# Kernel tuning notes

Measured on AMD Instinct MI355X. Metric: run time of the kernel, lower is better.

Reference implementation:

```python
import jax, jax.numpy as jnp
import numpy as np

EMB = 64          # emb_size
LG = 64           # lg_msg_dim
NDB = 16          # num_dist_basis
NCB = 16          # num_cos_basis
NCLS = 40
NLAYERS = 2
NJK = NLAYERS + 2  # jumping-knowledge sequence length
HID = (NJK * EMB) // 2  # PyG JK-LSTM hidden size = 128


def setup_inputs() -> dict:
    key = jax.random.key(0)
    ks = jax.random.split(key, 24)
    N, Eg, Elg, F = 50000, 800000, 800000, 128
    s = 0.05
    inp = {
        "x": jax.random.normal(ks[0], (N, F), jnp.float32),
        "edge_index_g": jax.random.randint(ks[1], (2, Eg), 0, N, jnp.int32),
        "edge_attr_g": jax.random.uniform(ks[2], (Eg, NDB), jnp.float32),
        "edge_index_lg": jax.random.randint(ks[3], (2, Elg), 0, Eg, jnp.int32),
        "edge_attr_lg": jax.random.uniform(ks[4], (Elg, NCB), jnp.float32),
        # parameters (nn.Linear convention: W is [out, in])
        "W_feat": jax.random.normal(ks[5], (EMB, F), jnp.float32) * s,
        "W_msg": jax.random.normal(ks[6], (LG, 2 * EMB + NDB), jnp.float32) * s,
        "W_lg2g": jax.random.normal(ks[7], (EMB, LG), jnp.float32) * s,
        "b_lg2g": jax.random.normal(ks[8], (EMB,), jnp.float32) * s,
        "W_msg_layers": jax.random.normal(ks[9], (NLAYERS, LG, 2 * LG + NCB), jnp.float32) * s,
        # bidirectional LSTM params (PyTorch gate order i,f,g,o)
        "Wih_f": jax.random.normal(ks[10], (4 * HID, EMB), jnp.float32) * s,
        "Whh_f": jax.random.normal(ks[11], (4 * HID, HID), jnp.float32) * s,
        "bih_f": jax.random.normal(ks[12], (4 * HID,), jnp.float32) * s,
        "bhh_f": jax.random.normal(ks[13], (4 * HID,), jnp.float32) * s,
        "Wih_b": jax.random.normal(ks[14], (4 * HID, EMB), jnp.float32) * s,
        "Whh_b": jax.random.normal(ks[15], (4 * HID, HID), jnp.float32) * s,
        "bih_b": jax.random.normal(ks[16], (4 * HID,), jnp.float32) * s,
        "bhh_b": jax.random.normal(ks[17], (4 * HID,), jnp.float32) * s,
        "W_att": jax.random.normal(ks[18], (1, 2 * HID), jnp.float32) * s,
        "b_att": jax.random.normal(ks[19], (1,), jnp.float32) * s,
        "W_out": jax.random.normal(ks[20], (NCLS, EMB), jnp.float32) * s,
    }
    return inp


def _lstm(x_seq, Wih, Whh, bih, bhh, reverse):
    # x_seq: [N, L, C] -> hs: [N, L, H]
    N = x_seq.shape[0]
    H = Whh.shape[1]
    b = bih + bhh

    def step(carry, x_t):
        h, c = carry
        gates = x_t @ Wih.T + h @ Whh.T + b
        i, f, g, o = jnp.split(gates, 4, axis=-1)
        c = jax.nn.sigmoid(f) * c + jax.nn.sigmoid(i) * jnp.tanh(g)
        h = jax.nn.sigmoid(o) * jnp.tanh(c)
        return (h, c), h

    xs = jnp.swapaxes(x_seq, 0, 1)  # [L, N, C]
    init = (jnp.zeros((N, H), x_seq.dtype), jnp.zeros((N, H), x_seq.dtype))
    _, hs = jax.lax.scan(step, init, xs, reverse=reverse)
    return jnp.swapaxes(hs, 0, 1)


def reference(x, edge_index_g, edge_attr_g, edge_index_lg, edge_attr_lg,
              W_feat, W_msg, W_lg2g, b_lg2g, W_msg_layers,
              Wih_f, Whh_f, bih_f, bhh_f, Wih_b, Whh_b, bih_b, bhh_b,
              W_att, b_att, W_out):
    N = x.shape[0]
    Eg = edge_attr_g.shape[0]
    seg = jax.ops.segment_sum

    # node embedding (eval mode: dropout is identity)
    node_emb = jax.nn.relu(x @ W_feat.T)  # [N, EMB]

    # initial linegraph node features: gather endpoints -> concat -> linear -> relu
    m1 = node_emb[edge_index_g[0]]  # [Eg, EMB]
    m2 = node_emb[edge_index_g[1]]
    msg_emb = jax.nn.relu(jnp.concatenate([m1, m2, edge_attr_g], -1) @ W_msg.T)  # [Eg, LG]

    node_embs = [node_emb]
    msg_red = msg_emb @ W_lg2g.T + b_lg2g
    node_embs.append(seg(msg_red, edge_index_g[1], num_segments=N))

    # message-passing layers on the linegraph
    for l in range(W_msg_layers.shape[0]):
        s = msg_emb[edge_index_lg[0]]
        d = msg_emb[edge_index_lg[1]]
        m = jax.nn.relu(jnp.concatenate([s, d, edge_attr_lg], -1) @ W_msg_layers[l].T)
        msg_emb = seg(m, edge_index_lg[1], num_segments=Eg)  # scatter_add over linegraph
        incoming = seg(msg_emb, edge_index_g[1], num_segments=N)
        node_embs.append(incoming @ W_lg2g.T + b_lg2g)

    # JumpingKnowledge ('lstm'): bidirectional LSTM -> attention -> weighted sum
    x_jk = jnp.stack(node_embs, axis=1)  # [N, NJK, EMB]
    h_f = _lstm(x_jk, Wih_f, Whh_f, bih_f, bhh_f, reverse=False)
    h_b = _lstm(x_jk, Wih_b, Whh_b, bih_b, bhh_b, reverse=True)
    h = jnp.concatenate([h_f, h_b], -1)  # [N, NJK, 2*HID]
    alpha = jax.nn.softmax((h @ W_att.T + b_att)[..., 0], axis=-1)  # [N, NJK]
    final_emb = jnp.sum(x_jk * alpha[..., None], axis=1)  # [N, EMB]

    out = final_emb @ W_out.T
    return jax.nn.log_softmax(out, axis=-1)
```

## Files before the change

### kernel.cpp

```cpp
#include <hip/hip_runtime.h>

typedef unsigned short u16;
typedef unsigned int u32;
typedef __attribute__((ext_vector_type(8))) short bf16x8;
typedef __attribute__((ext_vector_type(4))) float f32x4;

#define MFMA(a, b, c) __builtin_amdgcn_mfma_f32_16x16x32_bf16(a, b, c, 0, 0, 0)

__device__ __forceinline__ u16 f2bf(float x) {
    union { float f; u32 u; } v; v.f = x;
    u32 r = (v.u + 0x7FFFu + ((v.u >> 16) & 1u)) >> 16;
    return (u16)r;
}
__device__ __forceinline__ float bf2f(u16 b) {
    union { u32 u; float f; } v; v.u = ((u32)b) << 16;
    return v.f;
}
__device__ __forceinline__ void casAddPair(u32* w, float lo, float hi) {
    u32 old = *w, assumed;
    do {
        assumed = old;
        u32 des = (u32)f2bf(bf2f((u16)(assumed & 0xFFFFu)) + lo) |
                  ((u32)f2bf(bf2f((u16)(assumed >> 16)) + hi) << 16);
        if (des == assumed) break;
        old = atomicCAS(w, assumed, des);
    } while (old != assumed);
}

__global__ __launch_bounds__(256) void prep_w(
    const float* __restrict__ Whh_f, const float* __restrict__ Whh_b,
    const float* __restrict__ Wih_f, const float* __restrict__ Wih_b,
    const float* __restrict__ bih_f, const float* __restrict__ bhh_f,
    const float* __restrict__ bih_b, const float* __restrict__ bhh_b,
    const float* __restrict__ W_feat, const float* __restrict__ W_msg,
    const float* __restrict__ W_msg_l, const float* __restrict__ W_lg2g,
    u16* __restrict__ WhhB, u16* __restrict__ WihB, float* __restrict__ BS,
    u16* __restrict__ WfeatB, u16* __restrict__ WmsgB,
    u16* __restrict__ WmsgLB, u16* __restrict__ Wlg2gB)
{
    const float L2E = 1.4426950408889634f;
    int i = blockIdx.x * 256 + threadIdx.x;
    if (i < 131072) {
        int d = i >> 16, r = i & 65535;
        float s = (((r >> 14) & 3) == 2) ? 2.f * L2E : L2E;
        WhhB[i] = f2bf(s * (d ? Whh_b[r] : Whh_f[r]));
    } else if (i < 196608) {
        int i2 = i - 131072; int d = i2 >> 15, r = i2 & 32767;
        float s = (((r >> 13) & 3) == 2) ? 2.f * L2E : L2E;
        WihB[i2] = f2bf(s * (d ? Wih_b[r] : Wih_f[r]));
    } else if (i < 197632) {
        int i3 = i - 196608; int d = i3 >> 9, g = i3 & 511;
        float s = (((g >> 7) & 3) == 2) ? 2.f * L2E : L2E;
        BS[i3] = s * (d ? (bih_b[g] + bhh_b[g]) : (bih_f[g] + bhh_f[g]));
    } else if (i < 205824) {
        int j = i - 197632; WfeatB[j] = f2bf(W_feat[j]);
    } else if (i < 215040) {
        int j = i - 205824; WmsgB[j] = f2bf(W_msg[j]);
    } else if (i < 233472) {
        int j = i - 215040; WmsgLB[j] = f2bf(W_msg_l[j]);
    } else if (i < 237568) {
        int j = i - 233472; Wlg2gB[j] = f2bf(W_lg2g[j]);
    }
}

__global__ __launch_bounds__(256) void count_kernel(const int* __restrict__ dst,
                                                    u32* __restrict__ cnt, long E)
{
    long i = (long)blockIdx.x * 256 + threadIdx.x;
    if (i < E) atomicAdd(&cnt[dst[i]], 1u);
}

__global__ __launch_bounds__(256) void scan1(const u32* __restrict__ a,
                                             u32* __restrict__ part, int n)
{
    __shared__ u32 ts[256];
    int b = blockIdx.x, t = threadIdx.x;
    long i0 = (long)b * 1024 + t * 4;
    u32 s = 0;
#pragma unroll
    for (int k = 0; k < 4; ++k) { long i = i0 + k; if (i < n) s += a[i]; }
    ts[t] = s; __syncthreads();
    for (int off = 1; off < 256; off <<= 1) {
        u32 x = (t >= off) ? ts[t - off] : 0u;
        __syncthreads(); ts[t] += x; __syncthreads();
    }
    if (t == 255) part[b] = ts[255];
}

__global__ __launch_bounds__(1024) void scan2(u32* __restrict__ part, int nb,
                                              u32* __restrict__ total_out)
{
    __shared__ u32 ts[1024];
    int t = threadIdx.x;
    u32 v = (t < nb) ? part[t] : 0u;
    ts[t] = v; __syncthreads();
    for (int off = 1; off < 1024; off <<= 1) {
        u32 x = (t >= off) ? ts[t - off] : 0u;
        __syncthreads(); ts[t] += x; __syncthreads();
    }
    if (t < nb) part[t] = ts[t] - v;
    if (t == 1023 && total_out) *total_out = ts[1023];
}

__global__ __launch_bounds__(256) void scan3(u32* __restrict__ a,
                                             const u32* __restrict__ part, int n)
{
    __shared__ u32 ts[256];
    int b = blockIdx.x, t = threadIdx.x;
    long i0 = (long)b * 1024 + t * 4;
    u32 v[4]; u32 s = 0;
#pragma unroll
    for (int k = 0; k < 4; ++k) { long i = i0 + k; v[k] = (i < n) ? a[i] : 0u; s += v[k]; }
    ts[t] = s; __syncthreads();
    for (int off = 1; off < 256; off <<= 1) {
        u32 x = (t >= off) ? ts[t - off] : 0u;
        __syncthreads(); ts[t] += x; __syncthreads();
    }
    u32 run = part[b] + ts[t] - s;
#pragma unroll
    for (int k = 0; k < 4; ++k) {
        long i = i0 + k;
        if (i < n) { u32 x = v[k]; a[i] = run; run += x; }
    }
}

__global__ __launch_bounds__(256) void fill_kernel(const int* __restrict__ dst,
                                                   u32* __restrict__ off,
                                                   int* __restrict__ list, long E)
{
    long i = (long)blockIdx.x * 256 + threadIdx.x;
    if (i < E) {
        u32 pos = atomicAdd(&off[dst[i]], 1u);
        list[pos] = (int)i;
    }
}

__global__ __launch_bounds__(256) void zero_fill(const u32* __restrict__ offc,
                                                 u16* __restrict__ outb, long NB)
{
    long idx = (long)blockIdx.x * 256 + threadIdx.x;
    long n = idx >> 3; int q = (int)(idx & 7);
    if (n >= NB) return;
    u32 s = n ? offc[n - 1] : 0u;
    u32 e = offc[n];
    bool need = (s == e) || ((s >> 7) != ((e - 1) >> 7));
    if (need) *(uint4*)(outb + n * 64 + q * 8) = make_uint4(0, 0, 0, 0);
}

template <int K, bool RELU, bool INBF16>
__global__ __launch_bounds__(256) void rowgemm(
    const void* __restrict__ in, const u16* __restrict__ W,
    const float* __restrict__ bias, const float* __restrict__ bias_scale,
    u16* __restrict__ outb, int M)
{
    constexpr int KP = K + 8;
    constexpr int K8 = K / 8;
    __shared__ u16 inS[64 * KP];
    __shared__ u16 WS[64 * KP];
    int t = threadIdx.x;
    long rb = (long)blockIdx.x * 64;
    for (int i = t; i < 64 * K8; i += 256) {
        int c = i / K8, q = i - c * K8;
        *(uint4*)&WS[c * KP + q * 8] = *(const uint4*)&W[c * K + q * 8];
    }
    if (INBF16) {
        const u16* inb = (const u16*)in;
        for (int i = t; i < 64 * K8; i += 256) {
            int r = i / K8, q = i - r * K8;
            long gr = rb + r;
            uint4 v = make_uint4(0, 0, 0, 0);
            if (gr < M) v = *(const uint4*)&inb[gr * (long)K + q * 8];
            *(uint4*)&inS[r * KP + q * 8] = v;
        }
    } else {
        const float* inf = (const float*)in;
        for (int i = t; i < 64 * K; i += 256) {
            int r = i / K, k = i - r * K;
            long gr = rb + r;
            inS[r * KP + k] = (gr < M) ? f2bf(inf[gr * (long)K + k]) : (u16)0;
        }
    }
    __syncthreads();
    int l = t & 63, w = t >> 6, lr = l & 15, lq = l >> 4;
    f32x4 acc[4];
#pragma unroll
    for (int i = 0; i < 4; ++i) acc[i] = (f32x4){0.f, 0.f, 0.f, 0.f};
#pragma unroll
    for (int kc = 0; kc < K; kc += 32) {
        bf16x8 a = *(const bf16x8*)&inS[(w * 16 + lr) * KP + kc + lq * 8];
#pragma unroll
        for (int ct = 0; ct < 4; ++ct) {
            bf16x8 b = *(const bf16x8*)&WS[(ct * 16 + lr) * KP + kc + lq * 8];
            acc[ct] = MFMA(a, b, acc[ct]);
        }
    }
#pragma unroll
    for (int ct = 0; ct < 4; ++ct)
#pragma unroll
        for (int r = 0; r < 4; ++r) {
            long gr = rb + w * 16 + lq * 4 + r;
            if (gr < M) {
                int c = ct * 16 + lr;
                float v = acc[ct][r];
                if (bias) v += bias[c] * (bias_scale ? bias_scale[gr] : 1.f);
                if (RELU) v = fmaxf(v, 0.f);
                outb[gr * 64 + c] = f2bf(v);
            }
        }
}

__global__ __launch_bounds__(512, 4) void edge_msg_init2(
    const u16* __restrict__ feat, const int* __restrict__ ei,
    const float* __restrict__ attr, const u16* __restrict__ W,
    u16* __restrict__ outb, long E)
{
    __shared__ u16 WS[64 * 168];
    __shared__ u16 eds[128 * 64];
    int t = threadIdx.x;
    long eb = (long)blockIdx.x * 128;
    for (int i = t; i < 1152; i += 512) {
        int c = i / 18, q = i - c * 18;
        *(uint4*)&WS[c * 168 + q * 8] = *(const uint4*)&W[c * 144 + q * 8];
    }
    if (t < 192) {
        int c = t / 3, q = t - c * 3;
        *(uint4*)&WS[c * 168 + 144 + q * 8] = make_uint4(0, 0, 0, 0);
    }
    int w = t >> 6, l = t & 63, lr = l & 15, lq = l >> 4;
    long e = eb + w * 16 + lr;
    long ec = (e < E) ? e : (E - 1);
    int src = ei[ec], dst = ei[E + ec];
    bf16x8 A[5];
    {
        const uint4* sp = (const uint4*)(feat + (long)src * 64);
        const uint4* dp = (const uint4*)(feat + (long)dst * 64);
        *(uint4*)&A[0] = sp[lq];
        *(uint4*)&A[1] = sp[4 + lq];
        *(uint4*)&A[2] = dp[lq];
        *(uint4*)&A[3] = dp[4 + lq];
        uint4 pv = make_uint4(0, 0, 0, 0);
        if (lq < 2) {
            const float4* ap = (const float4*)(attr + ec * 16) + lq * 2;
            float4 b0 = ap[0], b1 = ap[1];
            pv.x = (u32)f2bf(b0.x) | ((u32)f2bf(b0.y) << 16);
            pv.y = (u32)f2bf(b0.z) | ((u32)f2bf(b0.w) << 16);
            pv.z = (u32)f2bf(b1.x) | ((u32)f2bf(b1.y) << 16);
            pv.w = (u32)f2bf(b1.z) | ((u32)f2bf(b1.w) << 16);
        }
        *(uint4*)&A[4] = pv;
    }
    __syncthreads();
    f32x4 acc[4];
#pragma unroll
    for (int ct = 0; ct < 4; ++ct) acc[ct] = (f32x4){0.f, 0.f, 0.f, 0.f};
#pragma unroll
    for (int kc = 0; kc < 5; ++kc) {
#pragma unroll
        for (int ct = 0; ct < 4; ++ct) {
            bf16x8 b = *(const bf16x8*)&WS[(ct * 16 + lr) * 168 + kc * 32 + lq * 8];
            acc[ct] = MFMA(A[kc], b, acc[ct]);
        }
    }
#pragma unroll
    for (int ct = 0; ct < 4; ++ct)
#pragma unroll
        for (int r = 0; r < 4; ++r) {
            int row = w * 16 + lq * 4 + r;
            int col = ct * 16 + lr;
            eds[row * 64 + col] = f2bf(fmaxf(acc[ct][r], 0.f));
        }
    __syncthreads();
    for (int j = t; j < 1024; j += 512) {
        int le = j >> 3, q = j & 7;
        long e2 = eb + le;
        if (e2 < E)
            *(uint4*)(outb + e2 * 64 + q * 8) = *(const uint4*)&eds[le * 64 + q * 8];
    }
}

__global__ __launch_bounds__(512, 4) void edge_msg_lg2(
    const u16* __restrict__ feat, const int* __restrict__ ei,
    const float* __restrict__ attr, const u16* __restrict__ W,
    const int* __restrict__ list, u16* __restrict__ outb, long E)
{
    __shared__ u16 WS[64 * 168];
    __shared__ u16 eds[128 * 64];
    __shared__ int dstS[128];
    __shared__ int idS[128];
    __shared__ int srcS[128];
    __shared__ int dprevS, dnextS;
    int t = threadIdx.x;
    long pb = (long)blockIdx.x * 128;
    for (int i = t; i < 1152; i += 512) {
        int c = i / 18, q = i - c * 18;
        *(uint4*)&WS[c * 168 + q * 8] = *(const uint4*)&W[c * 144 + q * 8];
    }
    if (t < 192) {
        int c = t / 3, q = t - c * 3;
        *(uint4*)&WS[c * 168 + 144 + q * 8] = make_uint4(0, 0, 0, 0);
    }
    if (t < 128) {
        long p = pb + t;
        int id = (p < E) ? list[p] : -1;
        idS[t] = id;
        srcS[t] = (id >= 0) ? ei[id] : 0;
        dstS[t] = (id >= 0) ? ei[E + id] : -1;
    } else if (t == 128) {
        dprevS = (pb > 0) ? ei[E + list[pb - 1]] : -2;
    } else if (t == 129) {
        dnextS = (pb + 128 < E) ? ei[E + list[pb + 128]] : -2;
    }
    __syncthreads();
    int w = t >> 6, l = t & 63, lr = l & 15, lq = l >> 4;
    int el = w * 16 + lr;
    int id = idS[el];
    long idc = (id >= 0) ? (long)id : 0;
    int src = srcS[el];
    int dst = (dstS[el] >= 0) ? dstS[el] : 0;
    bf16x8 A[5];
    {
        const uint4* sp = (const uint4*)(feat + (long)src * 64);
        const uint4* dp = (const uint4*)(feat + (long)dst * 64);
        *(uint4*)&A[0] = sp[lq];
        *(uint4*)&A[1] = sp[4 + lq];
        *(uint4*)&A[2] = dp[lq];
        *(uint4*)&A[3] = dp[4 + lq];
        uint4 pv = make_uint4(0, 0, 0, 0);
        if (lq < 2) {
            const float4* ap = (const float4*)(attr + idc * 16) + lq * 2;
            float4 b0 = ap[0], b1 = ap[1];
            pv.x = (u32)f2bf(b0.x) | ((u32)f2bf(b0.y) << 16);
            pv.y = (u32)f2bf(b0.z) | ((u32)f2bf(b0.w) << 16);
            pv.z = (u32)f2bf(b1.x) | ((u32)f2bf(b1.y) << 16);
            pv.w = (u32)f2bf(b1.z) | ((u32)f2bf(b1.w) << 16);
        }
        *(uint4*)&A[4] = pv;
    }
    f32x4 acc[4];
#pragma unroll
    for (int ct = 0; ct < 4; ++ct) acc[ct] = (f32x4){0.f, 0.f, 0.f, 0.f};
#pragma unroll
    for (int kc = 0; kc < 5; ++kc) {
#pragma unroll
        for (int ct = 0; ct < 4; ++ct) {
            bf16x8 b = *(const bf16x8*)&WS[(ct * 16 + lr) * 168 + kc * 32 + lq * 8];
            acc[ct] = MFMA(A[kc], b, acc[ct]);
        }
    }
#pragma unroll
    for (int ct = 0; ct < 4; ++ct)
#pragma unroll
        for (int r = 0; r < 4; ++r) {
            int row = w * 16 + lq * 4 + r;
            int col = ct * 16 + lr;
            eds[row * 64 + col] = f2bf(fmaxf(acc[ct][r], 0.f));
        }
    __syncthreads();
    for (int j = t; j < 4096; j += 512) {
        int le = j >> 5, wd = j & 31;
        int d = dstS[le];
        if (d < 0) continue;
        if (le > 0 && dstS[le - 1] == d) continue;
        float lo = 0.f, hi = 0.f;
        int le2 = le;
        do {
            u32 pair = *(const u32*)&eds[le2 * 64 + wd * 2];
            lo += bf2f((u16)(pair & 0xFFFFu));
            hi += bf2f((u16)(pair >> 16));
            ++le2;
        } while (le2 < 128 && dstS[le2] == d);
        bool bprev = (le == 0 && dprevS == d);
        bool bnext = (le2 == 128 && dnextS == d);
        u32* dw = (u32*)(outb + (long)d * 64 + wd * 2);
        if (bprev || bnext) {
            casAddPair(dw, lo, hi);
        } else {
            *dw = (u32)f2bf(lo) | ((u32)f2bf(hi) << 16);
        }
    }
}

__global__ __launch_bounds__(256) void gather_gw(
    const u16* __restrict__ m, const int* __restrict__ list,
    const u32* __restrict__ offc, const u16* __restrict__ Wg,
    const float* __restrict__ bias, int useDeg,
    u16* __restrict__ outb, int N)
{
    __shared__ u16 WS[64 * 66];
    __shared__ float aggS[4][64];
    __shared__ float degS[4];
    int t = threadIdx.x;
    for (int i = t; i < 4096; i += 256) {
        int r = i >> 6, k = i & 63;
        WS[k * 66 + r] = Wg[i];
    }
    int wv = t >> 6, l = t & 63, c = l & 31, half = l >> 5;
    long n = (long)blockIdx.x * 4 + wv;
    long nn = (n < N) ? n : (long)(N - 1);
    u32 start = nn ? offc[nn - 1] : 0u;
    u32 end = offc[nn];
    float s0 = 0.f, s1 = 0.f;
    for (u32 i = start + half; i < end; i += 2) {
        int e = list[i];
        u32 pair = *(const u32*)&m[(long)e * 64 + c * 2];
        s0 += bf2f((u16)(pair & 0xFFFFu));
        s1 += bf2f((u16)(pair >> 16));
    }
    s0 += __shfl_xor(s0, 32);
    s1 += __shfl_xor(s1, 32);
    if (half == 0) { aggS[wv][c * 2] = s0; aggS[wv][c * 2 + 1] = s1; }
    if (l == 0) degS[wv] = (float)(end - start);
    __syncthreads();
    float acc = 0.f;
#pragma unroll 8
    for (int k = 0; k < 64; ++k)
        acc += aggS[wv][k] * bf2f(WS[k * 66 + l]);
    float scale = useDeg ? degS[wv] : 1.f;
    acc += bias[l] * scale;
    if (n < N) outb[n * 64 + l] = f2bf(acc);
}

__global__ __launch_bounds__(512, 2) void lstm3(
    const u16* __restrict__ jkB, const u16* __restrict__ WhhB,
    const u16* __restrict__ WihB, const float* __restrict__ BS,
    const float* __restrict__ Watt, float* __restrict__ scores,
    int N)
{
    __shared__ u16 hS[64 * 136];
    __shared__ u16 xS[2][64 * 72];
    __shared__ float bsS[512];
    __shared__ float part[4 * 64 * 8];
    int t = threadIdx.x;
    int dir = blockIdx.y;
    int w = t >> 6, l = t & 63, lr = l & 15, lq = l >> 4;
    const u16* WhhD = WhhB + (long)dir * 65536;
    const u16* WihD = WihB + (long)dir * 32768;
    long n0 = (long)blockIdx.x * 64;
    int pn = t >> 3, pj = t & 7;
    long pgn = n0 + pn;

    {
        int tt0 = dir ? 3 : 0;
        uint4 v = make_uint4(0, 0, 0, 0);
        if (pgn < N) v = *(const uint4*)&jkB[((long)tt0 * N + pgn) * 64 + pj * 8];
        *(uint4*)&xS[0][pn * 72 + pj * 8] = v;
    }
    bsS[t] = BS[dir * 512 + t];

    int grow0 = w * 16 + lq * 4;
    bf16x8 Wh[4][4];
#pragma unroll
    for (int ty = 0; ty < 4; ++ty) {
        int g = ty * 128 + w * 16 + lr;
#pragma unroll
        for (int kc = 0; kc < 4; ++kc)
            Wh[ty][kc] = *(const bf16x8*)&WhhD[g * 128 + kc * 32 + lq * 8];
    }
    const u16* pWiBase = WihD + (w * 16 + lr) * 64 + lq * 8;
    float4 Wa4 = *(const float4*)&Watt[dir * 128 + grow0];
    float* scOut = scores + (long)dir * N * 4;

    float creg[4][4] = {};
    __syncthreads();

#pragma unroll 1
    for (int s = 0; s < 4; ++s) {
        int tt = dir ? (3 - s) : s;
        int cur = s & 1;
        uint4 xpre;
        if (s < 3) {
            int ttn = dir ? (2 - s) : (s + 1);
            xpre = make_uint4(0, 0, 0, 0);
            if (pgn < N) xpre = *(const uint4*)&jkB[((long)ttn * N + pgn) * 64 + pj * 8];
        }
        const u16* pW = pWiBase;
        asm volatile("" : "+v"(pW));
        float u[4][4];
        {
            bf16x8 wi0 = *(const bf16x8*)(pW);
            bf16x8 wi1 = *(const bf16x8*)(pW + 32);
            bf16x8 wg0 = *(const bf16x8*)(pW + 16384);
            bf16x8 wg1 = *(const bf16x8*)(pW + 16416);
            f32x4 bi = *(const f32x4*)&bsS[grow0];
            f32x4 bg = *(const f32x4*)&bsS[256 + grow0];
            f32x4 acc[2][4];
#pragma unroll
            for (int nt = 0; nt < 4; ++nt) { acc[0][nt] = bi; acc[1][nt] = bg; }
            if (s) {
#pragma unroll
                for (int kc = 0; kc < 4; ++kc) {
                    bf16x8 a[4];
#pragma unroll
                    for (int nt = 0; nt < 4; ++nt)
                        a[nt] = *(const bf16x8*)&hS[(nt * 16 + lr) * 136 + kc * 32 + lq * 8];
#pragma unroll
                    for (int nt = 0; nt < 4; ++nt) {
                        acc[0][nt] = MFMA(Wh[0][kc], a[nt], acc[0][nt]);
                        acc[1][nt] = MFMA(Wh[2][kc], a[nt], acc[1][nt]);
                    }
                }
            }
#pragma unroll
            for (int kc = 0; kc < 2; ++kc) {
                bf16x8 wi = kc ? wi1 : wi0;
                bf16x8 wg = kc ? wg1 : wg0;
                bf16x8 a[4];
#pragma unroll
                for (int nt = 0; nt < 4; ++nt)
                    a[nt] = *(const bf16x8*)&xS[cur][(nt * 16 + lr) * 72 + kc * 32 + lq * 8];
#pragma unroll
                for (int nt = 0; nt < 4; ++nt) {
                    acc[0][nt] = MFMA(wi, a[nt], acc[0][nt]);
                    acc[1][nt] = MFMA(wg, a[nt], acc[1][nt]);
                }
            }
#pragma unroll
            for (int nt = 0; nt < 4; ++nt)
#pragma unroll
                for (int r = 0; r < 4; ++r) {
                    float si = __builtin_amdgcn_rcpf(
                        1.f + __builtin_amdgcn_exp2f(-acc[0][nt][r]));
                    float tg = 2.f * __builtin_amdgcn_rcpf(
                        1.f + __builtin_amdgcn_exp2f(-acc[1][nt][r])) - 1.f;
                    u[nt][r] = si * tg;
                }
        }
        {
            bf16x8 wf0 = *(const bf16x8*)(pW + 8192);
            bf16x8 wf1 = *(const bf16x8*)(pW + 8224);
            bf16x8 wo0 = *(const bf16x8*)(pW + 24576);
            bf16x8 wo1 = *(const bf16x8*)(pW + 24608);
            f32x4 bfv = *(const f32x4*)&bsS[128 + grow0];
            f32x4 bov = *(const f32x4*)&bsS[384 + grow0];
            f32x4 acc[2][4];
#pragma unroll
            for (int nt = 0; nt < 4; ++nt) { acc[0][nt] = bfv; acc[1][nt] = bov; }
            if (s) {
#pragma unroll
                for (int kc = 0; kc < 4; ++kc) {
                    bf16x8 a[4];
#pragma unroll
                    for (int nt = 0; nt < 4; ++nt)
                        a[nt] = *(const bf16x8*)&hS[(nt * 16 + lr) * 136 + kc * 32 + lq * 8];
#pragma unroll
                    for (int nt = 0; nt < 4; ++nt) {
                        acc[0][nt] = MFMA(Wh[1][kc], a[nt], acc[0][nt]);
                        acc[1][nt] = MFMA(Wh[3][kc], a[nt], acc[1][nt]);
                    }
                }
            }
#pragma unroll
            for (int kc = 0; kc < 2; ++kc) {
                bf16x8 wf = kc ? wf1 : wf0;
                bf16x8 wo = kc ? wo1 : wo0;
                bf16x8 a[4];
#pragma unroll
                for (int nt = 0; nt < 4; ++nt)
                    a[nt] = *(const bf16x8*)&xS[cur][(nt * 16 + lr) * 72 + kc * 32 + lq * 8];
#pragma unroll
                for (int nt = 0; nt < 4; ++nt) {
                    acc[0][nt] = MFMA(wf, a[nt], acc[0][nt]);
                    acc[1][nt] = MFMA(wo, a[nt], acc[1][nt]);
                }
            }
            if (s) __syncthreads();
#pragma unroll
            for (int nt = 0; nt < 4; ++nt) {
                float hv[4];
#pragma unroll
                for (int r = 0; r < 4; ++r) {
                    float sf = __builtin_amdgcn_rcpf(
                        1.f + __builtin_amdgcn_exp2f(-acc[0][nt][r]));
                    float c = sf * creg[nt][r] + u[nt][r];
                    float so = __builtin_amdgcn_rcpf(
                        1.f + __builtin_amdgcn_exp2f(-acc[1][nt][r]));
                    float th = 2.f * __builtin_amdgcn_rcpf(
                        1.f + __builtin_amdgcn_exp2f(-2.8853900817779268f * c)) - 1.f;
                    creg[nt][r] = c;
                    hv[r] = so * th;
                }
                float p = hv[0] * Wa4.x + hv[1] * Wa4.y + hv[2] * Wa4.z + hv[3] * Wa4.w;
                p += __shfl_xor(p, 16);
                p += __shfl_xor(p, 32);
                if (lq == 0) part[(tt * 64 + nt * 16 + lr) * 8 + w] = p;
                if (s < 3) {
                    u32 p0, p1;
                    asm("v_cvt_pk_bf16_f32 %0, %1, %2" : "=v"(p0) : "v"(hv[0]), "v"(hv[1]));
                    asm("v_cvt_pk_bf16_f32 %0, %1, %2" : "=v"(p1) : "v"(hv[2]), "v"(hv[3]));
                    *(uint2*)&hS[(nt * 16 + lr) * 136 + grow0] = make_uint2(p0, p1);
                }
            }
        }
        if (s < 3) {
            *(uint4*)&xS[cur ^ 1][pn * 72 + pj * 8] = xpre;
            __syncthreads();
        }
    }
    __syncthreads();
    if (t < 256) {
        int tt = t >> 6, node = t & 63;
        long gn = n0 + node;
        if (gn < N) {
            const float4* pp = (const float4*)&part[(tt * 64 + node) * 8];
            float4 a = pp[0], b = pp[1];
            scOut[gn * 4 + tt] = a.x + a.y + a.z + a.w + b.x + b.y + b.z + b.w;
        }
    }
}

__global__ __launch_bounds__(256) void final_kernel(
    const u16* __restrict__ jkB, const float* __restrict__ scores,
    const float* __restrict__ Wout, float* __restrict__ out, int N)
{
    __shared__ float feS[4][64];
    int t = threadIdx.x, l = t & 63, w = t >> 6;
    long n = (long)blockIdx.x * 4 + w;
    bool ok = (n < N);
    long nn = ok ? n : (long)(N - 1);
    float sc[4];
#pragma unroll
    for (int tt = 0; tt < 4; ++tt)
        sc[tt] = scores[nn * 4 + tt] + scores[(long)N * 4 + nn * 4 + tt];
    float m = fmaxf(fmaxf(sc[0], sc[1]), fmaxf(sc[2], sc[3]));
    float e0 = __expf(sc[0] - m), e1 = __expf(sc[1] - m);
    float e2 = __expf(sc[2] - m), e3 = __expf(sc[3] - m);
    float den = e0 + e1 + e2 + e3;
    float a0 = e0 / den, a1 = e1 / den, a2 = e2 / den, a3 = e3 / den;
    float fe = a0 * bf2f(jkB[nn * 64 + l]) + a1 * bf2f(jkB[((long)N + nn) * 64 + l]) +
               a2 * bf2f(jkB[((long)2 * N + nn) * 64 + l]) +
               a3 * bf2f(jkB[((long)3 * N + nn) * 64 + l]);
    feS[w][l] = fe;
    __syncthreads();
    float logit = 0.f;
    if (l < 40)
        for (int c = 0; c < 64; ++c) logit += feS[w][c] * Wout[l * 64 + c];
    float v = (l < 40) ? logit : -1e30f;
    for (int off = 32; off; off >>= 1) v = fmaxf(v, __shfl_xor(v, off));
    float ex = (l < 40) ? __expf(logit - v) : 0.f;
    for (int off = 32; off; off >>= 1) ex += __shfl_xor(ex, off);
    if (ok && l < 40) out[n * 40 + l] = logit - v - __logf(ex);
}

extern "C" void kernel_launch(void* const* d_in, const int* in_sizes, int n_in,
                              void* d_out, int out_size, void* d_ws, size_t ws_size,
                              hipStream_t stream)
{
    const float* x        = (const float*)d_in[0];
    const int*   eig      = (const int*)d_in[1];
    const float* eag      = (const float*)d_in[2];
    const int*   eilg     = (const int*)d_in[3];
    const float* ealg     = (const float*)d_in[4];
    const float* W_feat   = (const float*)d_in[5];
    const float* W_msg    = (const float*)d_in[6];
    const float* W_lg2g   = (const float*)d_in[7];
    const float* b_lg2g   = (const float*)d_in[8];
    const float* W_msg_l  = (const float*)d_in[9];
    const float* Wih_f    = (const float*)d_in[10];
    const float* Whh_f    = (const float*)d_in[11];
    const float* bih_f    = (const float*)d_in[12];
    const float* bhh_f    = (const float*)d_in[13];
    const float* Wih_b    = (const float*)d_in[14];
    const float* Whh_b    = (const float*)d_in[15];
    const float* bih_b    = (const float*)d_in[16];
    const float* bhh_b    = (const float*)d_in[17];
    const float* W_att    = (const float*)d_in[18];
    const float* W_out    = (const float*)d_in[20];

    int  N   = in_sizes[0] / 128;
    long Eg  = in_sizes[1] / 2;
    long Elg = in_sizes[3] / 2;

    char* wp = (char*)d_ws;
    auto alloc = [&](size_t bytes) -> char* {
        char* p = wp; wp += (bytes + 255) & ~(size_t)255; return p;
    };
    u16*   jkB    = (u16*)  alloc((size_t)4 * N * 64 * 2);
    u16*   mA     = (u16*)  alloc((size_t)Eg * 64 * 2);
    u16*   mB     = (u16*)  alloc((size_t)Eg * 64 * 2);
    float* scores = (float*)alloc((size_t)2 * N * 4 * 4);
    u16*   WhhB   = (u16*)  alloc((size_t)2 * 65536 * 2);
    u16*   WihB   = (u16*)  alloc((size_t)2 * 32768 * 2);
    float* BS     = (float*)alloc((size_t)2 * 512 * 4);
    u16*   WfeatB = (u16*)  alloc((size_t)8192 * 2);
    u16*   WmsgB  = (u16*)  alloc((size_t)9216 * 2);
    u16*   WmsgLB = (u16*)  alloc((size_t)18432 * 2);
    u16*   Wlg2gB = (u16*)  alloc((size_t)4096 * 2);
    u32*   off_g  = (u32*)  alloc((size_t)(N + 1) * 4);
    int*   list_g = (int*)  alloc((size_t)Eg * 4);
    u32*   off_lg = (u32*)  alloc((size_t)(Eg + 1) * 4);
    int*   list_lg= (int*)  alloc((size_t)Elg * 4);
    u32*   part   = (u32*)  alloc((size_t)1024 * 4);

    prep_w<<<928, 256, 0, stream>>>(Whh_f, Whh_b, Wih_f, Wih_b,
                                    bih_f, bhh_f, bih_b, bhh_b,
                                    W_feat, W_msg, W_msg_l, W_lg2g,
                                    WhhB, WihB, BS,
                                    WfeatB, WmsgB, WmsgLB, Wlg2gB);
    hipMemsetAsync(off_g, 0, (size_t)(N + 1) * 4, stream);
    count_kernel<<<(int)((Eg + 255) / 256), 256, 0, stream>>>(eig + Eg, off_g, Eg);
    {
        int nb = (N + 1023) / 1024;
        scan1<<<nb, 256, 0, stream>>>(off_g, part, N);
        scan2<<<1, 1024, 0, stream>>>(part, nb, off_g + N);
        scan3<<<nb, 256, 0, stream>>>(off_g, part, N);
    }
    fill_kernel<<<(int)((Eg + 255) / 256), 256, 0, stream>>>(eig + Eg, off_g, list_g, Eg);
    hipMemsetAsync(off_lg, 0, (size_t)(Eg + 1) * 4, stream);
    count_kernel<<<(int)((Elg + 255) / 256), 256, 0, stream>>>(eilg + Elg, off_lg, Elg);
    {
        int nb = (int)((Eg + 1023) / 1024);
        scan1<<<nb, 256, 0, stream>>>(off_lg, part, (int)Eg);
        scan2<<<1, 1024, 0, stream>>>(part, nb, off_lg + Eg);
        scan3<<<nb, 256, 0, stream>>>(off_lg, part, (int)Eg);
    }
    fill_kernel<<<(int)((Elg + 255) / 256), 256, 0, stream>>>(eilg + Elg, off_lg, list_lg, Elg);

    rowgemm<128, true, false><<<(N + 63) / 64, 256, 0, stream>>>(
        x, WfeatB, nullptr, nullptr, jkB, N);
    edge_msg_init2<<<(int)((Eg + 127) / 128), 512, 0, stream>>>(
        jkB, eig, eag, WmsgB, mA, Eg);
    gather_gw<<<(N + 3) / 4, 256, 0, stream>>>(
        mA, list_g, off_g, Wlg2gB, b_lg2g, 1, jkB + (size_t)N * 64, N);
    zero_fill<<<(int)((Eg * 8 + 255) / 256), 256, 0, stream>>>(off_lg, mB, Eg);
    edge_msg_lg2<<<(int)((Elg + 127) / 128), 512, 0, stream>>>(
        mA, eilg, ealg, WmsgLB, list_lg, mB, Elg);
    gather_gw<<<(N + 3) / 4, 256, 0, stream>>>(
        mB, list_g, off_g, Wlg2gB, b_lg2g, 0, jkB + (size_t)2 * N * 64, N);
    zero_fill<<<(int)((Eg * 8 + 255) / 256), 256, 0, stream>>>(off_lg, mA, Eg);
    edge_msg_lg2<<<(int)((Elg + 127) / 128), 512, 0, stream>>>(
        mB, eilg, ealg, WmsgLB + 9216, list_lg, mA, Elg);
    gather_gw<<<(N + 3) / 4, 256, 0, stream>>>(
        mA, list_g, off_g, Wlg2gB, b_lg2g, 0, jkB + (size_t)3 * N * 64, N);
    {
        int ntiles = (N + 63) / 64;
        lstm3<<<dim3(ntiles, 2), 512, 0, stream>>>(
            jkB, WhhB, WihB, BS, W_att, scores, N);
    }
    final_kernel<<<(N + 3) / 4, 256, 0, stream>>>(
        jkB, scores, W_out, (float*)d_out, N);
}
```

Measured before the change: 1.065 ms.

## Stage LSTM input weights and all timesteps in LDS; unroll gather reduction

The JK-LSTM kernel now preloads all four timestep inputs and the whole input-to-hidden weight matrix into shared memory at kernel start. This replaces the per-step global reloads of Wih and the double-buffered prefetch of x. The extra LDS (about 74KB for WiS plus a larger xS) may limit the two blocks per CU that the launch bounds request. Separately, the segment-gather kernel unrolls its edge loop by four with independent accumulators, so more loads are in flight at once.

```diff
diff --git a/kernel.cpp b/kernel.cpp
--- a/kernel.cpp
+++ b/kernel.cpp
@@ -399,16 +399,31 @@
     long nn = (n < N) ? n : (long)(N - 1);
     u32 start = nn ? offc[nn - 1] : 0u;
     u32 end = offc[nn];
-    float s0 = 0.f, s1 = 0.f;
-    for (u32 i = start + half; i < end; i += 2) {
+    float s0 = 0.f, s1 = 0.f, s2 = 0.f, s3 = 0.f;
+    float t0 = 0.f, t1 = 0.f, t2 = 0.f, t3 = 0.f;
+    u32 i = start + half;
+    for (; i + 6 < end; i += 8) {
+        int e0 = list[i], e1 = list[i + 2], e2 = list[i + 4], e3 = list[i + 6];
+        u32 p0 = *(const u32*)&m[(long)e0 * 64 + c * 2];
+        u32 p1 = *(const u32*)&m[(long)e1 * 64 + c * 2];
+        u32 p2 = *(const u32*)&m[(long)e2 * 64 + c * 2];
+        u32 p3 = *(const u32*)&m[(long)e3 * 64 + c * 2];
+        s0 += bf2f((u16)(p0 & 0xFFFFu)); t0 += bf2f((u16)(p0 >> 16));
+        s1 += bf2f((u16)(p1 & 0xFFFFu)); t1 += bf2f((u16)(p1 >> 16));
+        s2 += bf2f((u16)(p2 & 0xFFFFu)); t2 += bf2f((u16)(p2 >> 16));
+        s3 += bf2f((u16)(p3 & 0xFFFFu)); t3 += bf2f((u16)(p3 >> 16));
+    }
+    for (; i < end; i += 2) {
         int e = list[i];
         u32 pair = *(const u32*)&m[(long)e * 64 + c * 2];
         s0 += bf2f((u16)(pair & 0xFFFFu));
-        s1 += bf2f((u16)(pair >> 16));
-    }
-    s0 += __shfl_xor(s0, 32);
-    s1 += __shfl_xor(s1, 32);
-    if (half == 0) { aggS[wv][c * 2] = s0; aggS[wv][c * 2 + 1] = s1; }
+        t0 += bf2f((u16)(pair >> 16));
+    }
+    float slo = (s0 + s1) + (s2 + s3);
+    float shi = (t0 + t1) + (t2 + t3);
+    slo += __shfl_xor(slo, 32);
+    shi += __shfl_xor(shi, 32);
+    if (half == 0) { aggS[wv][c * 2] = slo; aggS[wv][c * 2 + 1] = shi; }
     if (l == 0) degS[wv] = (float)(end - start);
     __syncthreads();
     float acc = 0.f;
@@ -427,7 +442,8 @@
     int N)
 {
     __shared__ u16 hS[64 * 136];
-    __shared__ u16 xS[2][64 * 72];
+    __shared__ u16 xS[4][64 * 72];
+    __shared__ u16 WiS[512 * 72];
     __shared__ float bsS[512];
     __shared__ float part[4 * 64 * 8];
     int t = threadIdx.x;
@@ -436,14 +452,21 @@
     const u16* WhhD = WhhB + (long)dir * 65536;
     const u16* WihD = WihB + (long)dir * 32768;
     long n0 = (long)blockIdx.x * 64;
-    int pn = t >> 3, pj = t & 7;
-    long pgn = n0 + pn;
 
     {
-        int tt0 = dir ? 3 : 0;
-        uint4 v = make_uint4(0, 0, 0, 0);
-        if (pgn < N) v = *(const uint4*)&jkB[((long)tt0 * N + pgn) * 64 + pj * 8];
-        *(uint4*)&xS[0][pn * 72 + pj * 8] = v;
+        int n = t >> 3, j = t & 7;
+        long gn = n0 + n;
+#pragma unroll
+        for (int k = 0; k < 4; ++k) {
+            uint4 v = make_uint4(0, 0, 0, 0);
+            if (gn < N) v = *(const uint4*)&jkB[((long)k * N + gn) * 64 + j * 8];
+            *(uint4*)&xS[k][n * 72 + j * 8] = v;
+        }
+    }
+#pragma unroll
+    for (int i = t; i < 4096; i += 512) {
+        int g = i >> 3, q = i & 7;
+        *(uint4*)&WiS[g * 72 + q * 8] = *(const uint4*)&WihD[g * 64 + q * 8];
     }
     bsS[t] = BS[dir * 512 + t];
 
@@ -456,7 +479,6 @@
         for (int kc = 0; kc < 4; ++kc)
             Wh[ty][kc] = *(const bf16x8*)&WhhD[g * 128 + kc * 32 + lq * 8];
     }
-    const u16* pWiBase = WihD + (w * 16 + lr) * 64 + lq * 8;
     float4 Wa4 = *(const float4*)&Watt[dir * 128 + grow0];
     float* scOut = scores + (long)dir * N * 4;
 
@@ -466,24 +488,11 @@
 #pragma unroll 1
     for (int s = 0; s < 4; ++s) {
         int tt = dir ? (3 - s) : s;
-        int cur = s & 1;
-        uint4 xpre;
-        if (s < 3) {
-            int ttn = dir ? (2 - s) : (s + 1);
-            xpre = make_uint4(0, 0, 0, 0);
-            if (pgn < N) xpre = *(const uint4*)&jkB[((long)ttn * N + pgn) * 64 + pj * 8];
-        }
-        const u16* pW = pWiBase;
-        asm volatile("" : "+v"(pW));
         float u[4][4];
         {
-            bf16x8 wi0 = *(const bf16x8*)(pW);
-            bf16x8 wi1 = *(const bf16x8*)(pW + 32);
-            bf16x8 wg0 = *(const bf16x8*)(pW + 16384);
-            bf16x8 wg1 = *(const bf16x8*)(pW + 16416);
+            f32x4 acc[2][4];
             f32x4 bi = *(const f32x4*)&bsS[grow0];
             f32x4 bg = *(const f32x4*)&bsS[256 + grow0];
-            f32x4 acc[2][4];
 #pragma unroll
             for (int nt = 0; nt < 4; ++nt) { acc[0][nt] = bi; acc[1][nt] = bg; }
             if (s) {
@@ -502,12 +511,12 @@
             }
 #pragma unroll
             for (int kc = 0; kc < 2; ++kc) {
-                bf16x8 wi = kc ? wi1 : wi0;
-                bf16x8 wg = kc ? wg1 : wg0;
+                bf16x8 wi = *(const bf16x8*)&WiS[(w * 16 + lr) * 72 + kc * 32 + lq * 8];
+                bf16x8 wg = *(const bf16x8*)&WiS[(256 + w * 16 + lr) * 72 + kc * 32 + lq * 8];
                 bf16x8 a[4];
 #pragma unroll
                 for (int nt = 0; nt < 4; ++nt)
-                    a[nt] = *(const bf16x8*)&xS[cur][(nt * 16 + lr) * 72 + kc * 32 + lq * 8];
+                    a[nt] = *(const bf16x8*)&xS[tt][(nt * 16 + lr) * 72 + kc * 32 + lq * 8];
 #pragma unroll
                 for (int nt = 0; nt < 4; ++nt) {
                     acc[0][nt] = MFMA(wi, a[nt], acc[0][nt]);
@@ -526,15 +535,11 @@
                 }
         }
         {
-            bf16x8 wf0 = *(const bf16x8*)(pW + 8192);
-            bf16x8 wf1 = *(const bf16x8*)(pW + 8224);
-            bf16x8 wo0 = *(const bf16x8*)(pW + 24576);
-            bf16x8 wo1 = *(const bf16x8*)(pW + 24608);
-            f32x4 bfv = *(const f32x4*)&bsS[128 + grow0];
-            f32x4 bov = *(const f32x4*)&bsS[384 + grow0];
             f32x4 acc[2][4];
-#pragma unroll
-            for (int nt = 0; nt < 4; ++nt) { acc[0][nt] = bfv; acc[1][nt] = bov; }
+            f32x4 bf = *(const f32x4*)&bsS[128 + grow0];
+            f32x4 bo = *(const f32x4*)&bsS[384 + grow0];
+#pragma unroll
+            for (int nt = 0; nt < 4; ++nt) { acc[0][nt] = bf; acc[1][nt] = bo; }
             if (s) {
 #pragma unroll
                 for (int kc = 0; kc < 4; ++kc) {
@@ -551,12 +556,12 @@
             }
 #pragma unroll
             for (int kc = 0; kc < 2; ++kc) {
-                bf16x8 wf = kc ? wf1 : wf0;
-                bf16x8 wo = kc ? wo1 : wo0;
+                bf16x8 wf = *(const bf16x8*)&WiS[(128 + w * 16 + lr) * 72 + kc * 32 + lq * 8];
+                bf16x8 wo = *(const bf16x8*)&WiS[(384 + w * 16 + lr) * 72 + kc * 32 + lq * 8];
                 bf16x8 a[4];
 #pragma unroll
                 for (int nt = 0; nt < 4; ++nt)
-                    a[nt] = *(const bf16x8*)&xS[cur][(nt * 16 + lr) * 72 + kc * 32 + lq * 8];
+                    a[nt] = *(const bf16x8*)&xS[tt][(nt * 16 + lr) * 72 + kc * 32 + lq * 8];
 #pragma unroll
                 for (int nt = 0; nt < 4; ++nt) {
                     acc[0][nt] = MFMA(wf, a[nt], acc[0][nt]);
@@ -591,10 +596,7 @@
                 }
             }
         }
-        if (s < 3) {
-            *(uint4*)&xS[cur ^ 1][pn * 72 + pj * 8] = xpre;
-            __syncthreads();
-        }
+        if (s < 3) __syncthreads();
     }
     __syncthreads();
     if (t < 256) {
```

New measurement: 991.2 us (median of 2 runs). 6.9% less time.
